# Kernel tuning notes

Hardware: AMD Instinct MI355X
Metric: run time of the kernel (lower is better)

Reference implementation:

```python
import jax, jax.numpy as jnp
import numpy as np

B, T, C = 2, 2048, 2048
H, HK = 16, 4          # n_head, n_kv_head (GQA)
HD = C // H            # head_dim = 128
EPS = 1e-6             # rms-norm eps


def _rope(x, cos, sin):
    # x: [B,T,h,d]; cos/sin: [T, d/2] (rotate-half RoPE)
    d2 = x.shape[-1] // 2
    x1, x2 = x[..., :d2], x[..., d2:]
    c = cos[None, :, None, :]
    s = sin[None, :, None, :]
    return jnp.concatenate([x1 * c - x2 * s, x1 * s + x2 * c], axis=-1)


def _rms(x):
    # weightless QK-norm (F.rms_norm over last dim)
    return x * jax.lax.rsqrt(jnp.mean(x * x, axis=-1, keepdims=True) + EPS)


def setup_inputs() -> dict:
    key = jax.random.key(0)
    ks = jax.random.split(key, 6)
    x = jax.random.normal(ks[0], (B, T, C), dtype=jnp.float32)
    # realistic RoPE tables
    inv_freq = 1.0 / (10000.0 ** (jnp.arange(0, HD, 2, dtype=jnp.float32) / HD))  # [HD/2]
    ang = jnp.arange(T, dtype=jnp.float32)[:, None] * inv_freq[None, :]           # [T, HD/2]
    cos, sin = jnp.cos(ang), jnp.sin(ang)
    std = 0.02
    Wq = jax.random.normal(ks[1], (C, H * HD), dtype=jnp.float32) * std
    Wk = jax.random.normal(ks[2], (C, HK * HD), dtype=jnp.float32) * std
    Wv = jax.random.normal(ks[3], (C, HK * HD), dtype=jnp.float32) * std
    Wproj = jax.random.normal(ks[4], (C, C), dtype=jnp.float32) * std
    mix1 = jnp.float32(1.0)
    mix2 = jnp.float32(0.5)
    return {"x": x, "cos": cos, "sin": sin, "Wq": Wq, "Wk": Wk, "Wv": Wv,
            "Wproj": Wproj, "mix1": mix1, "mix2": mix2}


def reference(x, cos, sin, Wq, Wk, Wv, Wproj, mix1, mix2):
    Bx, Tx, Cx = x.shape
    q = (x @ Wq).reshape(Bx, Tx, H, HD)
    k = (x @ Wk).reshape(Bx, Tx, HK, HD)
    v = (x @ Wv).reshape(Bx, Tx, HK, HD)
    q = _rms(_rope(q, cos, sin))
    k = _rms(_rope(k, cos, sin))
    q = q.transpose(0, 2, 1, 3)  # [B,H,T,D]
    k = k.transpose(0, 2, 1, 3)  # [B,HK,T,D]
    v = v.transpose(0, 2, 1, 3)
    rep = H // HK
    k = jnp.repeat(k, rep, axis=1)  # GQA repeat -> [B,H,T,D]
    v = jnp.repeat(v, rep, axis=1)
    att = jnp.einsum('bhqd,bhkd->bhqk', q, k) * (1.0 / np.sqrt(HD))
    mask = jnp.tril(jnp.ones((Tx, Tx), dtype=bool))
    att = jnp.where(mask[None, None], att, -jnp.inf)
    att = jax.nn.softmax(att, axis=-1)
    y1 = att @ v            # first-order attention output
    y2 = att @ y1           # second-order simplicial mixing (reuses att)
    y = mix1 * y1 + mix2 * y2
    y = y.transpose(0, 2, 1, 3).reshape(Bx, Tx, Cx)
    return y @ Wproj
```

## Files before the change

### kernel.cpp

```cpp
#include <hip/hip_runtime.h>
#include <hip/hip_bf16.h>
#include <cstdint>
#include <cstddef>

#define AS1 __attribute__((address_space(1)))
#define AS3 __attribute__((address_space(3)))

typedef __attribute__((ext_vector_type(8))) short bf16x8;
typedef __attribute__((ext_vector_type(4))) float f32x4;

__device__ __forceinline__ void gload_lds16(const void* g, void* l) {
  __builtin_amdgcn_global_load_lds((const AS1 void*)g, (AS3 void*)l, 16, 0, 0);
}

#define MFMA_BF16(A, B, C) __builtin_amdgcn_mfma_f32_16x16x32_bf16((A), (B), (C), 0, 0, 0)

#define QSCALE 0.12751744f

__device__ __forceinline__ uint32_t pk2(float a, float b) {
  uint32_t ua = (uint32_t)__builtin_bit_cast(unsigned short, __float2bfloat16(a));
  uint32_t ub = (uint32_t)__builtin_bit_cast(unsigned short, __float2bfloat16(b));
  return ua | (ub << 16);
}
__device__ __forceinline__ float b2f(unsigned short u) {
  return __builtin_bit_cast(float, (uint32_t)u << 16);
}

__device__ __forceinline__ float red8_sum(float v) {
  int x;
  x = __builtin_amdgcn_update_dpp(0, __builtin_bit_cast(int, v), 0xB1, 0xF, 0xF, true);
  v += __builtin_bit_cast(float, x);
  x = __builtin_amdgcn_update_dpp(0, __builtin_bit_cast(int, v), 0x4E, 0xF, 0xF, true);
  v += __builtin_bit_cast(float, x);
  x = __builtin_amdgcn_update_dpp(0, __builtin_bit_cast(int, v), 0x141, 0xF, 0xF, true);
  v += __builtin_bit_cast(float, x);
  return v;
}

__global__ __launch_bounds__(256) void cast_bf16_kernel(const float* __restrict__ in,
                                                        __hip_bfloat16* __restrict__ out,
                                                        int n4) {
  int i = blockIdx.x * 256 + threadIdx.x;
  if (i < n4) {
    float4 v = ((const float4*)in)[i];
    __hip_bfloat16* o = out + (size_t)i * 4;
    o[0] = __float2bfloat16(v.x);
    o[1] = __float2bfloat16(v.y);
    o[2] = __float2bfloat16(v.z);
    o[3] = __float2bfloat16(v.w);
  }
}

__global__ __launch_bounds__(256) void wtrans_kernel(const float* __restrict__ Wq,
                                                     const float* __restrict__ Wk,
                                                     const float* __restrict__ Wv,
                                                     const float* __restrict__ Wp,
                                                     __hip_bfloat16* __restrict__ WTa,
                                                     __hip_bfloat16* __restrict__ WpT) {
  __shared__ float tile[32][33];
  int id = blockIdx.x;
  const float* in; __hip_bfloat16* out; int is, os, bx, by;
  if (id < 4096)      { in = Wq; out = WTa;                          is = 2048; os = 2048; bx = id & 63; by = id >> 6; }
  else if (id < 5120) { int t = id - 4096; in = Wk; out = WTa + (size_t)2048 * 2048; is = 512; os = 2048; bx = t & 15; by = t >> 4; }
  else if (id < 6144) { int t = id - 5120; in = Wv; out = WTa + (size_t)2560 * 2048; is = 512; os = 2048; bx = t & 15; by = t >> 4; }
  else                { int t = id - 6144; in = Wp; out = WpT;       is = 2048; os = 2048; bx = t & 63; by = t >> 6; }
  int c0 = bx * 32, r0 = by * 32;
  int tx = threadIdx.x, ty = threadIdx.y;
#pragma unroll
  for (int i = 0; i < 32; i += 8)
    tile[ty + i][tx] = in[(size_t)(r0 + ty + i) * is + c0 + tx];
  __syncthreads();
#pragma unroll
  for (int i = 0; i < 32; i += 8)
    out[(size_t)(c0 + ty + i) * os + r0 + tx] = __float2bfloat16(tile[tx][ty + i]);
}

__global__ __launch_bounds__(256) void gemm_qkv_rope_kernel(
    const __hip_bfloat16* __restrict__ A,
    const __hip_bfloat16* __restrict__ Bt,
    const float* __restrict__ cosb,
    const float* __restrict__ sinb,
    __hip_bfloat16* __restrict__ qT,
    __hip_bfloat16* __restrict__ kT,
    __hip_bfloat16* __restrict__ vt) {
  __shared__ __align__(16) char smem[34048];
  __hip_bfloat16* CL4 = (__hip_bfloat16*)smem;
  const int K = 2048;
  const int tid = threadIdx.x;
  const int lane = tid & 63;
  const int wid = tid >> 6;
  const int wm = wid >> 1, wn = wid & 1;
  const int nwg = gridDim.x;
  const int bid = blockIdx.x;
  const int swz = (bid & 7) * (nwg >> 3) + (bid >> 3);
  const int tm = swz / 24, tn = swz % 24;
  const int row0 = tm << 7, col0 = tn << 7;
  const int fr = lane & 15;
  const int hi = lane >> 4;
  const int kg = hi * 8;

  auto STAGE = [&](int buf, int k0) {
#pragma unroll
    for (int i = 0; i < 2; ++i) {
      int f = i * 256 + tid;
      int r = f >> 2, s = f & 3;
      gload_lds16(A + (size_t)(row0 + r) * K + k0 + s * 8,
                  smem + buf * 8192 + (i * 256 + wid * 64) * 16);
      gload_lds16(Bt + (size_t)(col0 + r) * K + k0 + s * 8,
                  smem + 16384 + buf * 8192 + (i * 256 + wid * 64) * 16);
    }
  };

  f32x4 acc[4][4] = {};
  STAGE(0, 0);
  int cur = 0;
  for (int kk = 0; kk < 64; ++kk) {
    if (kk > 0) __builtin_amdgcn_s_barrier();
    __builtin_amdgcn_sched_barrier(0);
    if (kk + 1 < 64) STAGE(cur ^ 1, (kk + 1) * 32);
    __builtin_amdgcn_sched_barrier(0);
    if (kk + 1 < 64) asm volatile("s_waitcnt vmcnt(4)" ::: "memory");
    else             asm volatile("s_waitcnt vmcnt(0)" ::: "memory");
    __builtin_amdgcn_s_barrier();
    __builtin_amdgcn_sched_barrier(0);
    const __hip_bfloat16* Ac = (const __hip_bfloat16*)(smem + cur * 8192);
    const __hip_bfloat16* Bc = (const __hip_bfloat16*)(smem + 16384 + cur * 8192);
    bf16x8 af[4], bfr[4];
#pragma unroll
    for (int m = 0; m < 4; ++m)
      af[m] = *(const bf16x8*)(Ac + (wm * 64 + m * 16 + fr) * 32 + kg);
#pragma unroll
    for (int n = 0; n < 4; ++n)
      bfr[n] = *(const bf16x8*)(Bc + (wn * 64 + n * 16 + fr) * 32 + kg);
#pragma unroll
    for (int m = 0; m < 4; ++m)
#pragma unroll
      for (int n = 0; n < 4; ++n)
        acc[m][n] = MFMA_BF16(af[m], bfr[n], acc[m][n]);
    cur ^= 1;
  }
  __syncthreads();

#pragma unroll
  for (int m = 0; m < 4; ++m)
#pragma unroll
    for (int n = 0; n < 4; ++n) {
      int q4 = wm * 16 + m * 4 + hi;
      int col = wn * 64 + n * 16 + fr;
      *(uint2*)(CL4 + ((q4 * 133 + col) << 2)) =
          make_uint2(pk2(acc[m][n][0], acc[m][n][1]), pk2(acc[m][n][2], acc[m][n][3]));
    }
  __syncthreads();

  const int b = row0 >> 11;
  const int t0 = row0 & 2047;

  if (col0 >= 2560) {
    const int hv = (col0 - 2560) >> 7;
    __hip_bfloat16* vb = vt + (size_t)(b * 4 + hv) * 128 * 2048;
    const int col = tid >> 1, th = tid & 1;
    uint2 w[16];
#pragma unroll
    for (int qq = 0; qq < 16; ++qq)
      w[qq] = *(const uint2*)(CL4 + (((th * 16 + qq) * 133 + col) << 2));
    __hip_bfloat16* dstv = vb + (size_t)col * 2048 + t0 + th * 64;
#pragma unroll
    for (int e = 0; e < 8; ++e)
      *(uint4*)(dstv + e * 8) = make_uint4(w[2 * e].x, w[2 * e].y, w[2 * e + 1].x, w[2 * e + 1].y);
    return;
  }

  const int quad = tid >> 3, cp = tid & 7;
  const int tb = t0 + quad * 4;
  bf16x8 lov[4], hiv[4];
#pragma unroll
  for (int e = 0; e < 4; ++e) {
    lov[e] = *(const bf16x8*)(CL4 + ((quad * 133 + cp * 8 + e * 2) << 2));
    hiv[e] = *(const bf16x8*)(CL4 + ((quad * 133 + 64 + cp * 8 + e * 2) << 2));
  }
  const float oscale = (col0 < 2048) ? QSCALE : 1.0f;
  __hip_bfloat16* dstq = (col0 < 2048)
      ? qT + (size_t)(b * 16 + (col0 >> 7)) * 2048 * 128
      : kT + (size_t)(b * 4 + ((col0 - 2048) >> 7)) * 2048 * 128;

  float o1v[4][8], o2v[4][8], ssum[4];
#pragma unroll
  for (int rr = 0; rr < 4; ++rr) {
    const float* cb = cosb + (size_t)(tb + rr) * 64 + cp * 8;
    const float* sb = sinb + (size_t)(tb + rr) * 64 + cp * 8;
    float4 c0 = *(const float4*)cb, c1 = *(const float4*)(cb + 4);
    float4 s0 = *(const float4*)sb, s1 = *(const float4*)(sb + 4);
    float cc[8] = {c0.x, c0.y, c0.z, c0.w, c1.x, c1.y, c1.z, c1.w};
    float sn[8] = {s0.x, s0.y, s0.z, s0.w, s1.x, s1.y, s1.z, s1.w};
    float ss = 0.f;
#pragma unroll
    for (int e = 0; e < 4; ++e)
#pragma unroll
      for (int w2 = 0; w2 < 2; ++w2) {
        int pd = e * 2 + w2;
        float x1 = b2f((unsigned short)lov[e][w2 * 4 + rr]);
        float x2 = b2f((unsigned short)hiv[e][w2 * 4 + rr]);
        float a = x1 * cc[pd] - x2 * sn[pd];
        float bb = x1 * sn[pd] + x2 * cc[pd];
        o1v[rr][pd] = a;
        o2v[rr][pd] = bb;
        ss += a * a + bb * bb;
      }
    ssum[rr] = ss;
  }
#pragma unroll
  for (int rr = 0; rr < 4; ++rr) {
    float rn = rsqrtf(red8_sum(ssum[rr]) * (1.f / 128.f) + 1e-6f) * oscale;
    __hip_bfloat16* dr = dstq + (size_t)(tb + rr) * 128 + cp * 8;
    *(uint4*)dr = make_uint4(pk2(o1v[rr][0] * rn, o1v[rr][1] * rn),
                             pk2(o1v[rr][2] * rn, o1v[rr][3] * rn),
                             pk2(o1v[rr][4] * rn, o1v[rr][5] * rn),
                             pk2(o1v[rr][6] * rn, o1v[rr][7] * rn));
    *(uint4*)(dr + 64) = make_uint4(pk2(o2v[rr][0] * rn, o2v[rr][1] * rn),
                                    pk2(o2v[rr][2] * rn, o2v[rr][3] * rn),
                                    pk2(o2v[rr][4] * rn, o2v[rr][5] * rn),
                                    pk2(o2v[rr][6] * rn, o2v[rr][7] * rn));
  }
}

__global__ __launch_bounds__(256) void gemm_bf16_kernel(const __hip_bfloat16* __restrict__ A,
                                                        const __hip_bfloat16* __restrict__ Bt,
                                                        float* __restrict__ C,
                                                        int M, int N, int K) {
  __shared__ __align__(16) char smem[32768];
  const int tid = threadIdx.x;
  const int lane = tid & 63;
  const int wid = tid >> 6;
  const int wm = wid >> 1, wn = wid & 1;
  const int nwg = gridDim.x;
  const int bid = blockIdx.x;
  const int swz = (bid & 7) * (nwg >> 3) + (bid >> 3);
  const int ntile = N >> 7;
  const int tm = swz / ntile, tn = swz % ntile;
  const int row0 = tm << 7, col0 = tn << 7;

  const int fr = lane & 15;
  const int kg = (lane >> 4) * 8;

  auto STAGE = [&](int buf, int k0) {
#pragma unroll
    for (int i = 0; i < 2; ++i) {
      int f = i * 256 + tid;
      int r = f >> 2, s = f & 3;
      gload_lds16(A + (size_t)(row0 + r) * K + k0 + s * 8,
                  smem + buf * 8192 + (i * 256 + wid * 64) * 16);
      gload_lds16(Bt + (size_t)(col0 + r) * K + k0 + s * 8,
                  smem + 16384 + buf * 8192 + (i * 256 + wid * 64) * 16);
    }
  };

  f32x4 acc[4][4] = {};
  const int nk = K >> 5;
  STAGE(0, 0);
  int cur = 0;
  for (int kk = 0; kk < nk; ++kk) {
    if (kk > 0) __builtin_amdgcn_s_barrier();
    __builtin_amdgcn_sched_barrier(0);
    if (kk + 1 < nk) STAGE(cur ^ 1, (kk + 1) * 32);
    __builtin_amdgcn_sched_barrier(0);
    if (kk + 1 < nk) asm volatile("s_waitcnt vmcnt(4)" ::: "memory");
    else             asm volatile("s_waitcnt vmcnt(0)" ::: "memory");
    __builtin_amdgcn_s_barrier();
    __builtin_amdgcn_sched_barrier(0);
    const __hip_bfloat16* Ac = (const __hip_bfloat16*)(smem + cur * 8192);
    const __hip_bfloat16* Bc = (const __hip_bfloat16*)(smem + 16384 + cur * 8192);
    bf16x8 af[4], bfr[4];
#pragma unroll
    for (int m = 0; m < 4; ++m)
      af[m] = *(const bf16x8*)(Ac + (wm * 64 + m * 16 + fr) * 32 + kg);
#pragma unroll
    for (int n = 0; n < 4; ++n)
      bfr[n] = *(const bf16x8*)(Bc + (wn * 64 + n * 16 + fr) * 32 + kg);
#pragma unroll
    for (int m = 0; m < 4; ++m)
#pragma unroll
      for (int n = 0; n < 4; ++n)
        acc[m][n] = MFMA_BF16(af[m], bfr[n], acc[m][n]);
    cur ^= 1;
  }

  const int cr = (lane >> 4) * 4;
#pragma unroll
  for (int m = 0; m < 4; ++m)
#pragma unroll
    for (int n = 0; n < 4; ++n) {
      int col = col0 + wn * 64 + n * 16 + fr;
#pragma unroll
      for (int r = 0; r < 4; ++r) {
        int row = row0 + wm * 64 + m * 16 + cr + r;
        C[(size_t)row * N + col] = acc[m][n][r];
      }
    }
}


__global__ __launch_bounds__(256, 2) void attn_pass1_kernel(
    const __hip_bfloat16* __restrict__ qT,
    const __hip_bfloat16* __restrict__ kT,
    const __hip_bfloat16* __restrict__ vt,
    __hip_bfloat16* __restrict__ y1u,
    float* __restrict__ Mb,
    float* __restrict__ Lb,
    const float* __restrict__ mix1p,
    const float* __restrict__ mix2p) {
  __shared__ __align__(16) __hip_bfloat16 Ks[2][64 * 128];
  __shared__ __align__(16) __hip_bfloat16 Vs[2][128 * 64];
  __shared__ __align__(16) char Ps[4][32 * 128];
  const int tid = threadIdx.x, lane = tid & 63, wid = tid >> 6;
  const int bi = blockIdx.x;
  const int u = bi & 255, half = bi >> 8;
  const int g = u & 7;
  const int pslot = (u >> 3) & 7;
  const int bh = g * 4 + (u >> 6);
  const int j = half ? (15 - pslot) : pslot;
  const int q0 = j * 128;
  const int nt = 2 * j + 2;
  const int sd = 2 * j + (wid >> 1);
  const __hip_bfloat16* Kp = kT + (size_t)g * 2048 * 128;
  const __hip_bfloat16* Vp = vt + (size_t)g * 128 * 2048;
  const int fr = lane & 15, hi = lane >> 4;

  bf16x8 qf[2][4];
  {
    const __hip_bfloat16* Qp = qT + ((size_t)bh * 2048 + q0 + wid * 32) * 128;
#pragma unroll
    for (int rr = 0; rr < 2; ++rr)
#pragma unroll
      for (int dc = 0; dc < 4; ++dc)
        qf[rr][dc] = *(const bf16x8*)(Qp + (rr * 16 + fr) * 128 + dc * 32 + hi * 8);
  }

  f32x4 accO[2][8] = {};
  float m[2], l[2];
  m[0] = m[1] = -1e30f; l[0] = l[1] = 0.f;

  char* Pb = Ps[wid];

  auto STAGE = [&](int buf, int kt) {
    const int k0 = kt * 64;
#pragma unroll
    for (int i = 0; i < 4; ++i) {
      int f = i * 256 + tid;
      int r = f >> 4, s = f & 15, sx = s ^ (r & 7);
      gload_lds16(Kp + (size_t)(k0 + r) * 128 + sx * 8,
                  (char*)Ks[buf] + (i * 256 + wid * 64) * 16);
    }
#pragma unroll
    for (int i = 0; i < 4; ++i) {
      int f = i * 256 + tid;
      int r = f >> 3, s = f & 7, sx = s ^ (r & 7);
      gload_lds16(Vp + (size_t)r * 2048 + k0 + sx * 8,
                  (char*)Vs[buf] + (i * 256 + wid * 64) * 16);
    }
  };

  STAGE(0, 0);
  int cur = 0;
  for (int s = 0; s < nt; ++s) {
    if (s > 0) __builtin_amdgcn_s_barrier();
    __builtin_amdgcn_sched_barrier(0);
    if (s + 1 < nt) STAGE(cur ^ 1, s + 1);
    __builtin_amdgcn_sched_barrier(0);
    if (s + 1 < nt) asm volatile("s_waitcnt vmcnt(8)" ::: "memory");
    else            asm volatile("s_waitcnt vmcnt(0)" ::: "memory");
    __builtin_amdgcn_s_barrier();
    __builtin_amdgcn_sched_barrier(0);

    const bool active = (s <= sd);
    if (active) {
      const char* Kc = (const char*)Ks[cur];
      f32x4 sf[2][4] = {};
      __builtin_amdgcn_s_setprio(1);
#pragma unroll
      for (int c = 0; c < 4; ++c) {
        const int krow = c * 16 + fr;
#pragma unroll
        for (int dc = 0; dc < 4; ++dc) {
          int slot = (dc * 4 + hi) ^ (krow & 7);
          bf16x8 kf = *(const bf16x8*)(Kc + krow * 256 + slot * 16);
          sf[0][c] = MFMA_BF16(kf, qf[0][dc], sf[0][c]);
          sf[1][c] = MFMA_BF16(kf, qf[1][dc], sf[1][c]);
        }
      }
      __builtin_amdgcn_s_setprio(0);
      float rmax[2];
#pragma unroll
      for (int rr = 0; rr < 2; ++rr) {
        if (s == sd) {
          const int qq = q0 + wid * 32 + rr * 16 + fr;
#pragma unroll
          for (int c = 0; c < 4; ++c) {
            const int kb = s * 64 + c * 16 + hi * 4;
#pragma unroll
            for (int r = 0; r < 4; ++r)
              if (kb + r > qq) sf[rr][c][r] = -1e30f;
          }
        }
        float v = -1e30f;
#pragma unroll
        for (int c = 0; c < 4; ++c)
#pragma unroll
          for (int r = 0; r < 4; ++r) v = fmaxf(v, sf[rr][c][r]);
        v = fmaxf(v, __shfl_xor(v, 16));
        v = fmaxf(v, __shfl_xor(v, 32));
        rmax[rr] = v;
      }
      bool grow = (rmax[0] > m[0] + 8.f) | (rmax[1] > m[1] + 8.f);
      if (__any(grow)) {
        float a[2];
#pragma unroll
        for (int rr = 0; rr < 2; ++rr) {
          float mn = fmaxf(m[rr], rmax[rr]);
          a[rr] = __builtin_amdgcn_exp2f(m[rr] - mn);
          m[rr] = mn;
          l[rr] *= a[rr];
        }
#pragma unroll
        for (int rr = 0; rr < 2; ++rr)
#pragma unroll
          for (int r = 0; r < 4; ++r) {
            float aq = __shfl(a[rr], hi * 4 + r);
#pragma unroll
            for (int f = 0; f < 8; ++f) accO[rr][f][r] *= aq;
          }
      }
#pragma unroll
      for (int rr = 0; rr < 2; ++rr) {
        float rs = 0.f;
#pragma unroll
        for (int c = 0; c < 4; ++c)
#pragma unroll
          for (int r = 0; r < 4; ++r) {
            float p = __builtin_amdgcn_exp2f(sf[rr][c][r] - m[rr]);
            sf[rr][c][r] = p;
            rs += p;
          }
        rs += __shfl_xor(rs, 16);
        rs += __shfl_xor(rs, 32);
        l[rr] += rs;
      }
#pragma unroll
      for (int rr = 0; rr < 2; ++rr) {
        const int row = rr * 16 + fr;
        char* Prow = Pb + row * 128;
#pragma unroll
        for (int c = 0; c < 4; ++c) {
          uint32_t w0 = pk2(sf[rr][c][0], sf[rr][c][1]);
          uint32_t w1 = pk2(sf[rr][c][2], sf[rr][c][3]);
          int sl = (c * 2 + (hi >> 1)) ^ (row & 7);
          *(uint2*)(Prow + sl * 16 + (hi & 1) * 8) = make_uint2(w0, w1);
        }
      }
      bf16x8 pf[2][2];
#pragma unroll
      for (int rr = 0; rr < 2; ++rr) {
        const int row = rr * 16 + fr;
#pragma unroll
        for (int kc = 0; kc < 2; ++kc) {
          int sl = (kc * 4 + hi) ^ (row & 7);
          pf[rr][kc] = *(const bf16x8*)(Pb + row * 128 + sl * 16);
        }
      }
      const __hip_bfloat16* Vc = Vs[cur];
      __builtin_amdgcn_s_setprio(1);
#pragma unroll
      for (int kc = 0; kc < 2; ++kc)
#pragma unroll
        for (int f = 0; f < 8; ++f) {
          int vrow = f * 16 + fr;
          int vslot = (kc * 4 + hi) ^ (fr & 7);
          bf16x8 vf = *(const bf16x8*)(Vc + vrow * 64 + vslot * 8);
          accO[0][f] = MFMA_BF16(pf[0][kc], vf, accO[0][f]);
          accO[1][f] = MFMA_BF16(pf[1][kc], vf, accO[1][f]);
        }
      __builtin_amdgcn_s_setprio(0);
    }
    cur ^= 1;
  }

  const float m1v = mix1p[0], m2v = mix2p[0];
  float rlq[2][4];
#pragma unroll
  for (int rr = 0; rr < 2; ++rr) {
    float inv = 1.f / l[rr];
#pragma unroll
    for (int r = 0; r < 4; ++r) rlq[rr][r] = __shfl(inv, hi * 4 + r);
  }
  const int t0 = q0 + wid * 32;
#pragma unroll
  for (int rr = 0; rr < 2; ++rr) {
    const int tb = t0 + rr * 16 + hi * 4;
#pragma unroll
    for (int f = 0; f < 8; ++f) {
      const int d = f * 16 + fr;
      const ushort4 v4 = *(const ushort4*)(vt + ((size_t)g * 128 + d) * 2048 + tb);
      float u0 = m1v * b2f(v4.x) + m2v * (accO[rr][f][0] * rlq[rr][0]);
      float u1 = m1v * b2f(v4.y) + m2v * (accO[rr][f][1] * rlq[rr][1]);
      float u2 = m1v * b2f(v4.z) + m2v * (accO[rr][f][2] * rlq[rr][2]);
      float u3 = m1v * b2f(v4.w) + m2v * (accO[rr][f][3] * rlq[rr][3]);
      *(uint2*)(y1u + ((size_t)bh * 128 + d) * 2048 + tb) =
          make_uint2(pk2(u0, u1), pk2(u2, u3));
    }
  }
  if (hi == 0) {
#pragma unroll
    for (int rr = 0; rr < 2; ++rr) {
      Mb[(size_t)bh * 2048 + t0 + rr * 16 + fr] = m[rr];
      Lb[(size_t)bh * 2048 + t0 + rr * 16 + fr] = l[rr];
    }
  }
}

__global__ __launch_bounds__(256, 2) void attn_pass2_kernel(
    const __hip_bfloat16* __restrict__ qT,
    const __hip_bfloat16* __restrict__ kT,
    const __hip_bfloat16* __restrict__ y1u,
    const float* __restrict__ Mb,
    const float* __restrict__ Lb,
    __hip_bfloat16* __restrict__ ymix) {
  __shared__ __align__(16) __hip_bfloat16 Ks[2][64 * 128];
  __shared__ __align__(16) __hip_bfloat16 Vs[2][128 * 64];
  __shared__ __align__(16) char Ps[4][32 * 128];
  const int tid = threadIdx.x, lane = tid & 63, wid = tid >> 6;
  const int bi = blockIdx.x;
  const int u = bi & 255, half = bi >> 8;
  const int g = u & 7;
  const int pslot = (u >> 3) & 7;
  const int bh = g * 4 + (u >> 6);
  const int h = bh & 15, b = bh >> 4;
  const int j = half ? (15 - pslot) : pslot;
  const int q0 = j * 128;
  const int nt = 2 * j + 2;
  const int sd = 2 * j + (wid >> 1);
  const __hip_bfloat16* Kp = kT + (size_t)g * 2048 * 128;
  const __hip_bfloat16* Yp = y1u + (size_t)bh * 128 * 2048;
  const int fr = lane & 15, hi = lane >> 4;

  bf16x8 qf[2][4];
  float mr[2], rl[2];
  {
    const __hip_bfloat16* Qp = qT + ((size_t)bh * 2048 + q0 + wid * 32) * 128;
#pragma unroll
    for (int rr = 0; rr < 2; ++rr)
#pragma unroll
      for (int dc = 0; dc < 4; ++dc)
        qf[rr][dc] = *(const bf16x8*)(Qp + (rr * 16 + fr) * 128 + dc * 32 + hi * 8);
    const size_t qb = (size_t)bh * 2048 + q0 + wid * 32;
    mr[0] = Mb[qb + fr];        mr[1] = Mb[qb + 16 + fr];
    rl[0] = 1.f / Lb[qb + fr];  rl[1] = 1.f / Lb[qb + 16 + fr];
  }

  f32x4 accO[2][8] = {};
  char* Pb = Ps[wid];

  auto STAGE = [&](int buf, int kt) {
    const int k0 = kt * 64;
#pragma unroll
    for (int i = 0; i < 4; ++i) {
      int f = i * 256 + tid;
      int r = f >> 4, s = f & 15, sx = s ^ (r & 7);
      gload_lds16(Kp + (size_t)(k0 + r) * 128 + sx * 8,
                  (char*)Ks[buf] + (i * 256 + wid * 64) * 16);
    }
#pragma unroll
    for (int i = 0; i < 4; ++i) {
      int f = i * 256 + tid;
      int r = f >> 3, s = f & 7, sx = s ^ (r & 7);
      gload_lds16(Yp + (size_t)r * 2048 + k0 + sx * 8,
                  (char*)Vs[buf] + (i * 256 + wid * 64) * 16);
    }
  };

  STAGE(0, 0);
  int cur = 0;
  for (int s = 0; s < nt; ++s) {
    if (s > 0) __builtin_amdgcn_s_barrier();
    __builtin_amdgcn_sched_barrier(0);
    if (s + 1 < nt) STAGE(cur ^ 1, s + 1);
    __builtin_amdgcn_sched_barrier(0);
    if (s + 1 < nt) asm volatile("s_waitcnt vmcnt(8)" ::: "memory");
    else            asm volatile("s_waitcnt vmcnt(0)" ::: "memory");
    __builtin_amdgcn_s_barrier();
    __builtin_amdgcn_sched_barrier(0);

    const bool active = (s <= sd);
    if (active) {
      const char* Kc = (const char*)Ks[cur];
      f32x4 sf[2][4] = {};
      __builtin_amdgcn_s_setprio(1);
#pragma unroll
      for (int c = 0; c < 4; ++c) {
        const int krow = c * 16 + fr;
#pragma unroll
        for (int dc = 0; dc < 4; ++dc) {
          int slot = (dc * 4 + hi) ^ (krow & 7);
          bf16x8 kf = *(const bf16x8*)(Kc + krow * 256 + slot * 16);
          sf[0][c] = MFMA_BF16(kf, qf[0][dc], sf[0][c]);
          sf[1][c] = MFMA_BF16(kf, qf[1][dc], sf[1][c]);
        }
      }
      __builtin_amdgcn_s_setprio(0);
#pragma unroll
      for (int rr = 0; rr < 2; ++rr) {
        if (s == sd) {
          const int qq = q0 + wid * 32 + rr * 16 + fr;
#pragma unroll
          for (int c = 0; c < 4; ++c) {
            const int kb = s * 64 + c * 16 + hi * 4;
#pragma unroll
            for (int r = 0; r < 4; ++r)
              if (kb + r > qq) sf[rr][c][r] = -1e30f;
          }
        }
#pragma unroll
        for (int c = 0; c < 4; ++c)
#pragma unroll
          for (int r = 0; r < 4; ++r)
            sf[rr][c][r] = __builtin_amdgcn_exp2f(sf[rr][c][r] - mr[rr]) * rl[rr];
      }
#pragma unroll
      for (int rr = 0; rr < 2; ++rr) {
        const int row = rr * 16 + fr;
        char* Prow = Pb + row * 128;
#pragma unroll
        for (int c = 0; c < 4; ++c) {
          uint32_t w0 = pk2(sf[rr][c][0], sf[rr][c][1]);
          uint32_t w1 = pk2(sf[rr][c][2], sf[rr][c][3]);
          int sl = (c * 2 + (hi >> 1)) ^ (row & 7);
          *(uint2*)(Prow + sl * 16 + (hi & 1) * 8) = make_uint2(w0, w1);
        }
      }
      bf16x8 pf[2][2];
#pragma unroll
      for (int rr = 0; rr < 2; ++rr) {
        const int row = rr * 16 + fr;
#pragma unroll
        for (int kc = 0; kc < 2; ++kc) {
          int sl = (kc * 4 + hi) ^ (row & 7);
          pf[rr][kc] = *(const bf16x8*)(Pb + row * 128 + sl * 16);
        }
      }
      const __hip_bfloat16* Vc = Vs[cur];
      __builtin_amdgcn_s_setprio(1);
#pragma unroll
      for (int kc = 0; kc < 2; ++kc)
#pragma unroll
        for (int f = 0; f < 8; ++f) {
          int vrow = f * 16 + fr;
          int vslot = (kc * 4 + hi) ^ (fr & 7);
          bf16x8 vf = *(const bf16x8*)(Vc + vrow * 64 + vslot * 8);
          accO[0][f] = MFMA_BF16(pf[0][kc], vf, accO[0][f]);
          accO[1][f] = MFMA_BF16(pf[1][kc], vf, accO[1][f]);
        }
      __builtin_amdgcn_s_setprio(0);
    }
    cur ^= 1;
  }

#pragma unroll
  for (int rr = 0; rr < 2; ++rr) {
#pragma unroll
    for (int f = 0; f < 8; ++f) {
      const int d = f * 16 + fr;
#pragma unroll
      for (int r = 0; r < 4; ++r) {
        int q = q0 + wid * 32 + rr * 16 + hi * 4 + r;
        ymix[((size_t)b * 2048 + q) * 2048 + h * 128 + d] = __float2bfloat16(accO[rr][f][r]);
      }
    }
  }
}

extern "C" void kernel_launch(void* const* d_in, const int* in_sizes, int n_in,
                              void* d_out, int out_size, void* d_ws, size_t ws_size,
                              hipStream_t stream) {
  const float* x    = (const float*)d_in[0];
  const float* cosb = (const float*)d_in[1];
  const float* sinb = (const float*)d_in[2];
  const float* Wq   = (const float*)d_in[3];
  const float* Wk   = (const float*)d_in[4];
  const float* Wv   = (const float*)d_in[5];
  const float* Wp   = (const float*)d_in[6];
  const float* mix1 = (const float*)d_in[7];
  const float* mix2 = (const float*)d_in[8];
  float* out = (float*)d_out;
  char* ws = (char*)d_ws;

  __hip_bfloat16* xb   = (__hip_bfloat16*)(ws + 0);
  __hip_bfloat16* WTa  = (__hip_bfloat16*)(ws + 16777216);
  __hip_bfloat16* WpT  = (__hip_bfloat16*)(ws + 29360128);
  __hip_bfloat16* y1u  = (__hip_bfloat16*)(ws + 37748736);
  float*          Mb   = (float*)(ws + 54525952);
  float*          Lb   = (float*)(ws + 54788096);
  __hip_bfloat16* qTb  = (__hip_bfloat16*)(ws + 55050240);
  __hip_bfloat16* kTb  = (__hip_bfloat16*)(ws + 71827456);
  __hip_bfloat16* vtb  = (__hip_bfloat16*)(ws + 76021760);
  __hip_bfloat16* ymix = (__hip_bfloat16*)(ws + 0);

  dim3 tb(32, 8);
  cast_bf16_kernel<<<8192, 256, 0, stream>>>(x, xb, 2097152);
  wtrans_kernel<<<10240, tb, 0, stream>>>(Wq, Wk, Wv, Wp, WTa, WpT);

  gemm_qkv_rope_kernel<<<768, 256, 0, stream>>>(xb, WTa, cosb, sinb, qTb, kTb, vtb);

  attn_pass1_kernel<<<512, 256, 0, stream>>>(qTb, kTb, vtb, y1u, Mb, Lb, mix1, mix2);
  attn_pass2_kernel<<<512, 256, 0, stream>>>(qTb, kTb, y1u, Mb, Lb, ymix);

  gemm_bf16_kernel<<<512, 256, 0, stream>>>(ymix, WpT, out, 4096, 2048, 2048);
}
```

Measured before the change: 262.0 us.

## Enlarge QKV GEMM tile to 256x256 with 512 threads and swizzled LDS

The fused QKV+RoPE GEMM moves from 128x128 tiles with 256 threads to 256x256 tiles with 512 threads and BK=64. LDS staging gains an XOR swizzle to avoid bank conflicts, and MFMA issue is wrapped in setprio. The RoPE/norm and V-transpose epilogues are reworked for the wider tile. This raises data reuse per tile and cuts global traffic, but the grid shrinks to 192 blocks, which can underfill the 256 CUs, and LDS use grows to about 128KB per block.

```diff
diff --git a/kernel.cpp b/kernel.cpp
--- a/kernel.cpp
+++ b/kernel.cpp
@@ -25,14 +25,17 @@
 __device__ __forceinline__ float b2f(unsigned short u) {
   return __builtin_bit_cast(float, (uint32_t)u << 16);
 }
-
-__device__ __forceinline__ float red8_sum(float v) {
+__device__ __forceinline__ float elem4(uint2 w, int rr) {
+  uint32_t v = (rr & 2) ? w.y : w.x;
+  uint32_t u = (rr & 1) ? (v >> 16) : (v & 0xffffu);
+  return __builtin_bit_cast(float, u << 16);
+}
+
+__device__ __forceinline__ float red4_sum(float v) {
   int x;
   x = __builtin_amdgcn_update_dpp(0, __builtin_bit_cast(int, v), 0xB1, 0xF, 0xF, true);
   v += __builtin_bit_cast(float, x);
   x = __builtin_amdgcn_update_dpp(0, __builtin_bit_cast(int, v), 0x4E, 0xF, 0xF, true);
-  v += __builtin_bit_cast(float, x);
-  x = __builtin_amdgcn_update_dpp(0, __builtin_bit_cast(int, v), 0x141, 0xF, 0xF, true);
   v += __builtin_bit_cast(float, x);
   return v;
 }
@@ -75,7 +78,7 @@
     out[(size_t)(c0 + ty + i) * os + r0 + tx] = __float2bfloat16(tile[tx][ty + i]);
 }
 
-__global__ __launch_bounds__(256) void gemm_qkv_rope_kernel(
+__global__ __launch_bounds__(512, 2) void gemm_qkv_rope_kernel(
     const __hip_bfloat16* __restrict__ A,
     const __hip_bfloat16* __restrict__ Bt,
     const float* __restrict__ cosb,
@@ -83,71 +86,82 @@
     __hip_bfloat16* __restrict__ qT,
     __hip_bfloat16* __restrict__ kT,
     __hip_bfloat16* __restrict__ vt) {
-  __shared__ __align__(16) char smem[34048];
+  __shared__ __align__(16) char smem[131584];
   __hip_bfloat16* CL4 = (__hip_bfloat16*)smem;
   const int K = 2048;
   const int tid = threadIdx.x;
   const int lane = tid & 63;
   const int wid = tid >> 6;
-  const int wm = wid >> 1, wn = wid & 1;
-  const int nwg = gridDim.x;
+  const int wm = wid >> 2, wn = wid & 3;
   const int bid = blockIdx.x;
-  const int swz = (bid & 7) * (nwg >> 3) + (bid >> 3);
-  const int tm = swz / 24, tn = swz % 24;
-  const int row0 = tm << 7, col0 = tn << 7;
-  const int fr = lane & 15;
-  const int hi = lane >> 4;
-  const int kg = hi * 8;
+  const int swz = (bid & 7) * 24 + (bid >> 3);
+  const int tm = swz / 12, tn = swz % 12;
+  const int row0 = tm << 8, col0 = tn << 8;
+  const int fr = lane & 15, hi = lane >> 4;
 
   auto STAGE = [&](int buf, int k0) {
 #pragma unroll
-    for (int i = 0; i < 2; ++i) {
-      int f = i * 256 + tid;
-      int r = f >> 2, s = f & 3;
-      gload_lds16(A + (size_t)(row0 + r) * K + k0 + s * 8,
-                  smem + buf * 8192 + (i * 256 + wid * 64) * 16);
-      gload_lds16(Bt + (size_t)(col0 + r) * K + k0 + s * 8,
-                  smem + 16384 + buf * 8192 + (i * 256 + wid * 64) * 16);
+    for (int i = 0; i < 4; ++i) {
+      int f = i * 512 + tid;
+      int r = f >> 3, s = f & 7, sx = s ^ (r & 7);
+      gload_lds16(A + (size_t)(row0 + r) * K + k0 + sx * 8,
+                  smem + buf * 32768 + f * 16);
+    }
+#pragma unroll
+    for (int i = 0; i < 4; ++i) {
+      int f = i * 512 + tid;
+      int r = f >> 3, s = f & 7, sx = s ^ (r & 7);
+      gload_lds16(Bt + (size_t)(col0 + r) * K + k0 + sx * 8,
+                  smem + 65536 + buf * 32768 + f * 16);
     }
   };
 
-  f32x4 acc[4][4] = {};
+  f32x4 acc[8][4] = {};
   STAGE(0, 0);
   int cur = 0;
-  for (int kk = 0; kk < 64; ++kk) {
+  for (int kk = 0; kk < 32; ++kk) {
     if (kk > 0) __builtin_amdgcn_s_barrier();
     __builtin_amdgcn_sched_barrier(0);
-    if (kk + 1 < 64) STAGE(cur ^ 1, (kk + 1) * 32);
-    __builtin_amdgcn_sched_barrier(0);
-    if (kk + 1 < 64) asm volatile("s_waitcnt vmcnt(4)" ::: "memory");
+    if (kk + 1 < 32) STAGE(cur ^ 1, (kk + 1) * 64);
+    __builtin_amdgcn_sched_barrier(0);
+    if (kk + 1 < 32) asm volatile("s_waitcnt vmcnt(8)" ::: "memory");
     else             asm volatile("s_waitcnt vmcnt(0)" ::: "memory");
     __builtin_amdgcn_s_barrier();
     __builtin_amdgcn_sched_barrier(0);
-    const __hip_bfloat16* Ac = (const __hip_bfloat16*)(smem + cur * 8192);
-    const __hip_bfloat16* Bc = (const __hip_bfloat16*)(smem + 16384 + cur * 8192);
-    bf16x8 af[4], bfr[4];
-#pragma unroll
-    for (int m = 0; m < 4; ++m)
-      af[m] = *(const bf16x8*)(Ac + (wm * 64 + m * 16 + fr) * 32 + kg);
-#pragma unroll
-    for (int n = 0; n < 4; ++n)
-      bfr[n] = *(const bf16x8*)(Bc + (wn * 64 + n * 16 + fr) * 32 + kg);
-#pragma unroll
-    for (int m = 0; m < 4; ++m)
-#pragma unroll
-      for (int n = 0; n < 4; ++n)
-        acc[m][n] = MFMA_BF16(af[m], bfr[n], acc[m][n]);
+    const char* Ac = smem + cur * 32768;
+    const char* Bc = smem + 65536 + cur * 32768;
+#pragma unroll
+    for (int kh = 0; kh < 2; ++kh) {
+      bf16x8 bfr[4];
+#pragma unroll
+      for (int n = 0; n < 4; ++n) {
+        int rowb = wn * 64 + n * 16 + fr;
+        int sl = (kh * 4 + hi) ^ (rowb & 7);
+        bfr[n] = *(const bf16x8*)(Bc + rowb * 128 + sl * 16);
+      }
+      __builtin_amdgcn_s_setprio(1);
+#pragma unroll
+      for (int m = 0; m < 8; ++m) {
+        int rowa = wm * 128 + m * 16 + fr;
+        int sl = (kh * 4 + hi) ^ (rowa & 7);
+        bf16x8 af = *(const bf16x8*)(Ac + rowa * 128 + sl * 16);
+#pragma unroll
+        for (int n = 0; n < 4; ++n)
+          acc[m][n] = MFMA_BF16(af, bfr[n], acc[m][n]);
+      }
+      __builtin_amdgcn_s_setprio(0);
+    }
     cur ^= 1;
   }
   __syncthreads();
 
 #pragma unroll
-  for (int m = 0; m < 4; ++m)
+  for (int m = 0; m < 8; ++m)
 #pragma unroll
     for (int n = 0; n < 4; ++n) {
-      int q4 = wm * 16 + m * 4 + hi;
+      int q4 = wm * 32 + m * 4 + hi;
       int col = wn * 64 + n * 16 + fr;
-      *(uint2*)(CL4 + ((q4 * 133 + col) << 2)) =
+      *(uint2*)(CL4 + ((q4 * 257 + col) << 2)) =
           make_uint2(pk2(acc[m][n][0], acc[m][n][1]), pk2(acc[m][n][2], acc[m][n][3]));
     }
   __syncthreads();
@@ -155,71 +169,71 @@
   const int b = row0 >> 11;
   const int t0 = row0 & 2047;
 
-  if (col0 >= 2560) {
-    const int hv = (col0 - 2560) >> 7;
-    __hip_bfloat16* vb = vt + (size_t)(b * 4 + hv) * 128 * 2048;
+  if (tn >= 10) {
     const int col = tid >> 1, th = tid & 1;
-    uint2 w[16];
-#pragma unroll
-    for (int qq = 0; qq < 16; ++qq)
-      w[qq] = *(const uint2*)(CL4 + (((th * 16 + qq) * 133 + col) << 2));
-    __hip_bfloat16* dstv = vb + (size_t)col * 2048 + t0 + th * 64;
-#pragma unroll
-    for (int e = 0; e < 8; ++e)
-      *(uint4*)(dstv + e * 8) = make_uint4(w[2 * e].x, w[2 * e].y, w[2 * e + 1].x, w[2 * e + 1].y);
+    const int hv = ((col0 - 2560) >> 7) + (col >> 7);
+    const int d = col & 127;
+    __hip_bfloat16* dstv = vt + ((size_t)(b * 4 + hv) * 128 + d) * 2048 + t0 + th * 128;
+    uint2 w[32];
+#pragma unroll
+    for (int qq = 0; qq < 32; ++qq)
+      w[qq] = *(const uint2*)(CL4 + (((th * 32 + qq) * 257 + col) << 2));
+#pragma unroll
+    for (int e = 0; e < 16; ++e)
+      *(uint4*)(dstv + e * 8) =
+          make_uint4(w[2 * e].x, w[2 * e].y, w[2 * e + 1].x, w[2 * e + 1].y);
     return;
   }
 
   const int quad = tid >> 3, cp = tid & 7;
+  const int hh = cp >> 2, sub = cp & 3;
+  const float oscale = (tn < 8) ? QSCALE : 1.0f;
+  __hip_bfloat16* headbuf;
+  if (tn < 8) headbuf = qT + (size_t)(b * 16 + 2 * tn + hh) * 2048 * 128;
+  else        headbuf = kT + (size_t)(b * 4 + ((col0 - 2048) >> 7) + hh) * 2048 * 128;
+
+  uint2 lo[16], hi2[16];
+#pragma unroll
+  for (int jj = 0; jj < 16; ++jj) {
+    int colL = hh * 128 + sub * 16 + jj;
+    lo[jj]  = *(const uint2*)(CL4 + ((quad * 257 + colL) << 2));
+    hi2[jj] = *(const uint2*)(CL4 + ((quad * 257 + colL + 64) << 2));
+  }
   const int tb = t0 + quad * 4;
-  bf16x8 lov[4], hiv[4];
-#pragma unroll
-  for (int e = 0; e < 4; ++e) {
-    lov[e] = *(const bf16x8*)(CL4 + ((quad * 133 + cp * 8 + e * 2) << 2));
-    hiv[e] = *(const bf16x8*)(CL4 + ((quad * 133 + 64 + cp * 8 + e * 2) << 2));
-  }
-  const float oscale = (col0 < 2048) ? QSCALE : 1.0f;
-  __hip_bfloat16* dstq = (col0 < 2048)
-      ? qT + (size_t)(b * 16 + (col0 >> 7)) * 2048 * 128
-      : kT + (size_t)(b * 4 + ((col0 - 2048) >> 7)) * 2048 * 128;
-
-  float o1v[4][8], o2v[4][8], ssum[4];
 #pragma unroll
   for (int rr = 0; rr < 4; ++rr) {
-    const float* cb = cosb + (size_t)(tb + rr) * 64 + cp * 8;
-    const float* sb = sinb + (size_t)(tb + rr) * 64 + cp * 8;
-    float4 c0 = *(const float4*)cb, c1 = *(const float4*)(cb + 4);
-    float4 s0 = *(const float4*)sb, s1 = *(const float4*)(sb + 4);
-    float cc[8] = {c0.x, c0.y, c0.z, c0.w, c1.x, c1.y, c1.z, c1.w};
-    float sn[8] = {s0.x, s0.y, s0.z, s0.w, s1.x, s1.y, s1.z, s1.w};
+    const float* cb = cosb + (size_t)(tb + rr) * 64 + sub * 16;
+    const float* sb = sinb + (size_t)(tb + rr) * 64 + sub * 16;
+    float cc[16], sn[16];
+#pragma unroll
+    for (int e = 0; e < 4; ++e) {
+      float4 c4 = *(const float4*)(cb + e * 4);
+      float4 s4 = *(const float4*)(sb + e * 4);
+      cc[e * 4 + 0] = c4.x; cc[e * 4 + 1] = c4.y; cc[e * 4 + 2] = c4.z; cc[e * 4 + 3] = c4.w;
+      sn[e * 4 + 0] = s4.x; sn[e * 4 + 1] = s4.y; sn[e * 4 + 2] = s4.z; sn[e * 4 + 3] = s4.w;
+    }
+    float o1[16], o2[16];
     float ss = 0.f;
 #pragma unroll
-    for (int e = 0; e < 4; ++e)
-#pragma unroll
-      for (int w2 = 0; w2 < 2; ++w2) {
-        int pd = e * 2 + w2;
-        float x1 = b2f((unsigned short)lov[e][w2 * 4 + rr]);
-        float x2 = b2f((unsigned short)hiv[e][w2 * 4 + rr]);
-        float a = x1 * cc[pd] - x2 * sn[pd];
-        float bb = x1 * sn[pd] + x2 * cc[pd];
-        o1v[rr][pd] = a;
-        o2v[rr][pd] = bb;
-        ss += a * a + bb * bb;
-      }
-    ssum[rr] = ss;
-  }
-#pragma unroll
-  for (int rr = 0; rr < 4; ++rr) {
-    float rn = rsqrtf(red8_sum(ssum[rr]) * (1.f / 128.f) + 1e-6f) * oscale;
-    __hip_bfloat16* dr = dstq + (size_t)(tb + rr) * 128 + cp * 8;
-    *(uint4*)dr = make_uint4(pk2(o1v[rr][0] * rn, o1v[rr][1] * rn),
-                             pk2(o1v[rr][2] * rn, o1v[rr][3] * rn),
-                             pk2(o1v[rr][4] * rn, o1v[rr][5] * rn),
-                             pk2(o1v[rr][6] * rn, o1v[rr][7] * rn));
-    *(uint4*)(dr + 64) = make_uint4(pk2(o2v[rr][0] * rn, o2v[rr][1] * rn),
-                                    pk2(o2v[rr][2] * rn, o2v[rr][3] * rn),
-                                    pk2(o2v[rr][4] * rn, o2v[rr][5] * rn),
-                                    pk2(o2v[rr][6] * rn, o2v[rr][7] * rn));
+    for (int jj = 0; jj < 16; ++jj) {
+      float x1 = elem4(lo[jj], rr);
+      float x2 = elem4(hi2[jj], rr);
+      float a = x1 * cc[jj] - x2 * sn[jj];
+      float bb = x1 * sn[jj] + x2 * cc[jj];
+      o1[jj] = a; o2[jj] = bb;
+      ss += a * a + bb * bb;
+    }
+    ss = red4_sum(ss);
+    float rn = rsqrtf(ss * (1.f / 128.f) + 1e-6f) * oscale;
+    __hip_bfloat16* dr = headbuf + (size_t)(tb + rr) * 128 + sub * 16;
+    *(uint4*)dr = make_uint4(pk2(o1[0] * rn, o1[1] * rn), pk2(o1[2] * rn, o1[3] * rn),
+                             pk2(o1[4] * rn, o1[5] * rn), pk2(o1[6] * rn, o1[7] * rn));
+    *(uint4*)(dr + 8) = make_uint4(pk2(o1[8] * rn, o1[9] * rn), pk2(o1[10] * rn, o1[11] * rn),
+                                   pk2(o1[12] * rn, o1[13] * rn), pk2(o1[14] * rn, o1[15] * rn));
+    *(uint4*)(dr + 64) = make_uint4(pk2(o2[0] * rn, o2[1] * rn), pk2(o2[2] * rn, o2[3] * rn),
+                                    pk2(o2[4] * rn, o2[5] * rn), pk2(o2[6] * rn, o2[7] * rn));
+    *(uint4*)(dr + 72) = make_uint4(pk2(o2[8] * rn, o2[9] * rn), pk2(o2[10] * rn, o2[11] * rn),
+                                    pk2(o2[12] * rn, o2[13] * rn), pk2(o2[14] * rn, o2[15] * rn));
   }
 }
 
@@ -706,7 +720,7 @@
   cast_bf16_kernel<<<8192, 256, 0, stream>>>(x, xb, 2097152);
   wtrans_kernel<<<10240, tb, 0, stream>>>(Wq, Wk, Wv, Wp, WTa, WpT);
 
-  gemm_qkv_rope_kernel<<<768, 256, 0, stream>>>(xb, WTa, cosb, sinb, qTb, kTb, vtb);
+  gemm_qkv_rope_kernel<<<192, 512, 0, stream>>>(xb, WTa, cosb, sinb, qTb, kTb, vtb);
 
   attn_pass1_kernel<<<512, 256, 0, stream>>>(qTb, kTb, vtb, y1u, Mb, Lb, mix1, mix2);
   attn_pass2_kernel<<<512, 256, 0, stream>>>(qTb, kTb, y1u, Mb, Lb, ymix);
```

New measurement: 259.1 us. No clear change (-1.1%).
